# Kernel optimization log

Measured on AMD Instinct MI355X. Metric: run time of the kernel, lower is better.

## Reference

```python
import jax, jax.numpy as jnp
import numpy as np

SHAPELET_SIZE = 64
NUM_SHAPELETS = 128
IN_CHANNELS = 8


def setup_inputs() -> dict:
    key = jax.random.key(0)
    k1, k2 = jax.random.split(key)
    x = jax.random.normal(k1, (64, IN_CHANNELS, 2048), dtype=jnp.float32)
    shapelets = jax.random.normal(k2, (IN_CHANNELS, NUM_SHAPELETS, SHAPELET_SIZE), dtype=jnp.float32)
    return {"x": x, "shapelets": shapelets}


def _znorm(s):
    # Z-normalize along the time-step axis (dim 2), matching Znormalize_dim(shapelets, 2)
    mu = jnp.mean(s, axis=2, keepdims=True)
    sd = jnp.std(s, axis=2, keepdims=True)
    return (s - mu) / sd


def reference(x, shapelets):
    # x: (N, C, L); shapelets: (C, K, S)
    S = shapelets.shape[-1]
    N, C, L = x.shape
    W = L - S + 1
    # unfold(2, S, 1): sliding windows -> (N, C, W, S)
    idx = jnp.arange(W)[:, None] + jnp.arange(S)[None, :]  # (W, S)
    xw = x[:, :, idx]  # (N, C, W, S)
    sh = _znorm(shapelets)  # (C, K, S)
    # Euclidean cdist via ||a||^2 + ||b||^2 - 2 a.b (avoids (N,C,W,K,S) blowup)
    sq_x = jnp.sum(xw * xw, axis=-1)          # (N, C, W)
    sq_s = jnp.sum(sh * sh, axis=-1)          # (C, K)
    cross = jnp.einsum('ncws,cks->ncwk', xw, sh)  # (N, C, W, K)
    d2 = sq_x[..., None] + sq_s[None, :, None, :] - 2.0 * cross
    d = jnp.sqrt(jnp.maximum(d2, 1e-12))      # (N, C, W, K)
    # sum over channels, then global min over windows -> (N, 1, K)
    dsum = jnp.sum(d, axis=1)                 # (N, W, K)
    out = jnp.min(dsum, axis=1)[:, None, :]   # (N, 1, K)
    return out
```

## Files before the change

kernel.cpp:

```cpp
#include <hip/hip_runtime.h>
#include <math.h>

#define C 8
#define K 128
#define S 64
#define L 2048
#define NB 64
#define W (L - S + 1)
#define TW 128
#define NTW 16
#define XCS 200
#define XFS 200

typedef __attribute__((ext_vector_type(8))) short bf16x8;
typedef __attribute__((ext_vector_type(4))) float f32x4;

__device__ __forceinline__ unsigned short f2bf(float f) {
  unsigned int u = __float_as_uint(f);
  u += 0x7FFFu + ((u >> 16) & 1u);
  return (unsigned short)(u >> 16);
}

__global__ __launch_bounds__(256) void prep_kernel(const float* __restrict__ sh,
                                                   unsigned short* __restrict__ shzB,
                                                   float* __restrict__ sqs,
                                                   float* __restrict__ out) {
  int tid = blockIdx.x * 256 + threadIdx.x;
  if (tid < NB * K) out[tid] = __int_as_float(0x7F800000);
  int gid = blockIdx.x * 4 + (threadIdx.x >> 6);
  int lane = threadIdx.x & 63;
  float v = sh[(size_t)gid * S + lane];
  float s1 = v, s2 = v * v;
#pragma unroll
  for (int off = 32; off > 0; off >>= 1) {
    s1 += __shfl_down(s1, off);
    s2 += __shfl_down(s2, off);
  }
  s1 = __shfl(s1, 0);
  s2 = __shfl(s2, 0);
  float mu = s1 * (1.0f / S);
  float sd = sqrtf(fmaxf(s2 * (1.0f / S) - mu * mu, 0.0f));
  float z = (v - mu) / sd;
  int c = gid >> 7, k = gid & (K - 1), s = lane;
  int idx = c * 8192 + ((k >> 4) * 2 + (s >> 5)) * 512 +
            ((((s >> 3) & 3) * 16 + (k & 15)) * 8) + (s & 7);
  shzB[idx] = f2bf(z);
  float z2 = z * z;
#pragma unroll
  for (int off = 32; off > 0; off >>= 1) z2 += __shfl_down(z2, off);
  if (lane == 0) sqs[gid] = z2;
}

__global__ __launch_bounds__(256, 2) void main_kernel(const float* __restrict__ x,
                                                      const unsigned short* __restrict__ shzB,
                                                      const float* __restrict__ sqs,
                                                      int* __restrict__ out) {
  __shared__ __align__(16) unsigned short bbuf[2][8192];
  __shared__ __align__(16) unsigned short xcop[C][8][XCS];
  __shared__ __align__(16) float sqx[C][TW];

  const int t = threadIdx.x;
  const int lane = t & 63;
  const int wave = t >> 6;
  const int wgrp = wave >> 1;
  const int kgrp = wave & 1;
  const int col = lane & 15;
  const int quad = lane >> 4;
  const int n = blockIdx.y;
  const int w0 = blockIdx.x * TW;
  const float* xn = x + (size_t)n * C * L;

  {
    const unsigned short* g = shzB + t * 8;
    unsigned short* lb = &bbuf[0][wave * 512];
#pragma unroll
    for (int i = 0; i < 4; ++i)
      __builtin_amdgcn_global_load_lds(
          (const __attribute__((address_space(1))) void*)(g + i * 2048),
          (__attribute__((address_space(3))) void*)(lb + i * 2048), 16, 0, 0);
  }

  float* xf = (float*)&bbuf[1][0];
#pragma unroll
  for (int j = 0; j < 7; ++j) {
    int s = j * 256 + t;
    if (s < C * XFS) {
      int c = s / XFS, e = s - c * XFS;
      int g = w0 + e;
      xf[s] = (e < 192 && g < L) ? xn[c * L + g] : 0.0f;
    }
  }
  __syncthreads();

  {
    const int r = t >> 5, q = t & 31;
#pragma unroll
    for (int c = 0; c < C; ++c) {
#pragma unroll
      for (int j = 0; j < 3; ++j) {
        int i = (q + j * 32) * 2;
        int e = i + r;
        float f0 = xf[c * XFS + e];
        float f1 = xf[c * XFS + e + 1];
        unsigned int pk = (unsigned int)f2bf(f0) | ((unsigned int)f2bf(f1) << 16);
        *(unsigned int*)&xcop[c][r][i] = pk;
      }
    }
  }
  {
    int c = t >> 5, wl0 = (t & 31) << 2;
    const float* xr = xf + c * XFS;
    float s = 0.0f;
#pragma unroll
    for (int si = 0; si < S; ++si) { float v = xr[wl0 + si]; s = fmaf(v, v, s); }
    sqx[c][wl0] = s;
#pragma unroll
    for (int q = 1; q < 4; ++q) {
      float a = xr[wl0 + S - 1 + q], b = xr[wl0 + q - 1];
      s += a * a - b * b;
      sqx[c][wl0 + q] = s;
    }
  }
  __syncthreads();

  const f32x4 z4 = {0.0f, 0.0f, 0.0f, 0.0f};
  f32x4 dsum[4][4];
#pragma unroll
  for (int a = 0; a < 4; ++a)
#pragma unroll
    for (int b = 0; b < 4; ++b) dsum[a][b] = z4;

  const int m = col;
  const int r = m & 7;

  for (int c = 0; c < C; ++c) {
    if (c + 1 < C) {
      const unsigned short* g = shzB + (c + 1) * 8192 + t * 8;
      unsigned short* lb = &bbuf[(c + 1) & 1][wave * 512];
#pragma unroll
      for (int i = 0; i < 4; ++i)
        __builtin_amdgcn_global_load_lds(
            (const __attribute__((address_space(1))) void*)(g + i * 2048),
            (__attribute__((address_space(3))) void*)(lb + i * 2048), 16, 0, 0);
    }
    const unsigned short* bb = bbuf[c & 1];
    const unsigned short* xc = &xcop[c][0][0];

    f32x4 acc[4][4];
#pragma unroll
    for (int a = 0; a < 4; ++a)
#pragma unroll
      for (int b = 0; b < 4; ++b) acc[a][b] = z4;

#pragma unroll
    for (int ks = 0; ks < 2; ++ks) {
      bf16x8 bfr[4], afr[4];
#pragma unroll
      for (int kt = 0; kt < 4; ++kt)
        bfr[kt] = *(const bf16x8*)(bb + ((kgrp * 4 + kt) * 2 + ks) * 512 + lane * 8);
#pragma unroll
      for (int wt = 0; wt < 4; ++wt) {
        int i0 = wgrp * 64 + wt * 16 + m + ks * 32 + quad * 8 - r;
        afr[wt] = *(const bf16x8*)(xc + r * XCS + i0);
      }
#pragma unroll
      for (int wt = 0; wt < 4; ++wt)
#pragma unroll
        for (int kt = 0; kt < 4; ++kt)
          acc[wt][kt] = __builtin_amdgcn_mfma_f32_16x16x32_bf16(afr[wt], bfr[kt], acc[wt][kt], 0, 0, 0);
    }

    float sqsv[4];
#pragma unroll
    for (int kt = 0; kt < 4; ++kt) sqsv[kt] = sqs[c * K + kgrp * 64 + kt * 16 + col];
#pragma unroll
    for (int wt = 0; wt < 4; ++wt) {
      f32x4 sx = *(const f32x4*)&sqx[c][wgrp * 64 + wt * 16 + quad * 4];
#pragma unroll
      for (int kt = 0; kt < 4; ++kt) {
#pragma unroll
        for (int i = 0; i < 4; ++i) {
          float pre = sx[i] + sqsv[kt];
          float d2 = fmaf(-2.0f, acc[wt][kt][i], pre);
          dsum[wt][kt][i] += __builtin_amdgcn_sqrtf(fmaxf(d2, 1e-12f));
        }
      }
    }
    __syncthreads();
  }

  const float INF = __int_as_float(0x7F800000);
  int wbase = w0 + wgrp * 64;
#pragma unroll
  for (int kt = 0; kt < 4; ++kt) {
    float mv = INF;
#pragma unroll
    for (int wt = 0; wt < 4; ++wt)
#pragma unroll
      for (int i = 0; i < 4; ++i) {
        int w = wbase + wt * 16 + quad * 4 + i;
        float v = dsum[wt][kt][i];
        mv = (w < W) ? fminf(mv, v) : mv;
      }
    mv = fminf(mv, __shfl_xor(mv, 16));
    mv = fminf(mv, __shfl_xor(mv, 32));
    if (quad == 0)
      atomicMin(&out[n * K + kgrp * 64 + kt * 16 + col], __float_as_int(mv));
  }
}

extern "C" void kernel_launch(void* const* d_in, const int* in_sizes, int n_in,
                              void* d_out, int out_size, void* d_ws, size_t ws_size,
                              hipStream_t stream) {
  const float* x = (const float*)d_in[0];
  const float* sh = (const float*)d_in[1];
  float* out = (float*)d_out;
  unsigned short* shzB = (unsigned short*)d_ws;
  float* sqs = (float*)((char*)d_ws + C * K * S * 2);

  prep_kernel<<<256, 256, 0, stream>>>(sh, shzB, sqs, out);
  main_kernel<<<dim3(NTW, NB), 256, 0, stream>>>(x, shzB, sqs, (int*)out);
}
```

Measured before the change: 98.13 us.

## Load shapelet fragments from global into registers, widen blocks to 512 threads

Measured after the change: 187.2 us. +90.8%, slower.

```diff
diff --git a/kernel.cpp b/kernel.cpp
--- a/kernel.cpp
+++ b/kernel.cpp
@@ -44,168 +44,147 @@
   int c = gid >> 7, k = gid & (K - 1), s = lane;
   int idx = c * 8192 + ((k >> 4) * 2 + (s >> 5)) * 512 +
             ((((s >> 3) & 3) * 16 + (k & 15)) * 8) + (s & 7);
-  shzB[idx] = f2bf(z);
+  shzB[idx] = f2bf(-2.0f * z);
   float z2 = z * z;
 #pragma unroll
   for (int off = 32; off > 0; off >>= 1) z2 += __shfl_down(z2, off);
   if (lane == 0) sqs[gid] = z2;
 }
 
-__global__ __launch_bounds__(256, 2) void main_kernel(const float* __restrict__ x,
+__global__ __launch_bounds__(512, 4) void main_kernel(const float* __restrict__ x,
                                                       const unsigned short* __restrict__ shzB,
                                                       const float* __restrict__ sqs,
                                                       int* __restrict__ out) {
-  __shared__ __align__(16) unsigned short bbuf[2][8192];
   __shared__ __align__(16) unsigned short xcop[C][8][XCS];
   __shared__ __align__(16) float sqx[C][TW];
+  __shared__ __align__(16) float xf[C][XFS];
+  __shared__ __align__(16) float sqsl[C * K];
 
   const int t = threadIdx.x;
   const int lane = t & 63;
   const int wave = t >> 6;
-  const int wgrp = wave >> 1;
-  const int kgrp = wave & 1;
+  const int wgrp = wave & 1;
+  const int kgrp = wave >> 1;
   const int col = lane & 15;
   const int quad = lane >> 4;
   const int n = blockIdx.y;
   const int w0 = blockIdx.x * TW;
   const float* xn = x + (size_t)n * C * L;
 
-  {
-    const unsigned short* g = shzB + t * 8;
-    unsigned short* lb = &bbuf[0][wave * 512];
-#pragma unroll
-    for (int i = 0; i < 4; ++i)
-      __builtin_amdgcn_global_load_lds(
-          (const __attribute__((address_space(1))) void*)(g + i * 2048),
-          (__attribute__((address_space(3))) void*)(lb + i * 2048), 16, 0, 0);
-  }
-
-  float* xf = (float*)&bbuf[1][0];
-#pragma unroll
-  for (int j = 0; j < 7; ++j) {
-    int s = j * 256 + t;
+#pragma unroll
+  for (int j = 0; j < 4; ++j) {
+    int s = j * 512 + t;
     if (s < C * XFS) {
       int c = s / XFS, e = s - c * XFS;
       int g = w0 + e;
-      xf[s] = (e < 192 && g < L) ? xn[c * L + g] : 0.0f;
-    }
-  }
+      ((float*)xf)[s] = (e < 192 && g < L) ? xn[c * L + g] : 0.0f;
+    }
+  }
+  sqsl[t] = sqs[t];
+  sqsl[t + 512] = sqs[t + 512];
   __syncthreads();
 
   {
-    const int r = t >> 5, q = t & 31;
+    const int q = lane, r = wave;
 #pragma unroll
     for (int c = 0; c < C; ++c) {
-#pragma unroll
-      for (int j = 0; j < 3; ++j) {
-        int i = (q + j * 32) * 2;
-        int e = i + r;
-        float f0 = xf[c * XFS + e];
-        float f1 = xf[c * XFS + e + 1];
-        unsigned int pk = (unsigned int)f2bf(f0) | ((unsigned int)f2bf(f1) << 16);
+      {
+        int i = q * 2;
+        unsigned int pk = (unsigned int)f2bf(xf[c][i + r]) |
+                          ((unsigned int)f2bf(xf[c][i + r + 1]) << 16);
         *(unsigned int*)&xcop[c][r][i] = pk;
       }
+      if (q < 32) {
+        int i = 128 + q * 2;
+        unsigned int pk = (unsigned int)f2bf(xf[c][i + r]) |
+                          ((unsigned int)f2bf(xf[c][i + r + 1]) << 16);
+        *(unsigned int*)&xcop[c][r][i] = pk;
+      }
     }
   }
   {
-    int c = t >> 5, wl0 = (t & 31) << 2;
-    const float* xr = xf + c * XFS;
-    float s = 0.0f;
-#pragma unroll
-    for (int si = 0; si < S; ++si) { float v = xr[wl0 + si]; s = fmaf(v, v, s); }
-    sqx[c][wl0] = s;
-#pragma unroll
-    for (int q = 1; q < 4; ++q) {
-      float a = xr[wl0 + S - 1 + q], b = xr[wl0 + q - 1];
-      s += a * a - b * b;
-      sqx[c][wl0 + q] = s;
-    }
+    int c = t >> 6, wl = (t & 63) * 2;
+    const float* xr = xf[c];
+    float s0 = 0.0f;
+#pragma unroll
+    for (int si = 0; si < S; ++si) { float v = xr[wl + si]; s0 = fmaf(v, v, s0); }
+    sqx[c][wl] = s0;
+    float a = xr[wl + S], b = xr[wl];
+    sqx[c][wl + 1] = s0 + a * a - b * b;
   }
   __syncthreads();
 
   const f32x4 z4 = {0.0f, 0.0f, 0.0f, 0.0f};
-  f32x4 dsum[4][4];
+  f32x4 dsum[4][2];
 #pragma unroll
   for (int a = 0; a < 4; ++a)
 #pragma unroll
-    for (int b = 0; b < 4; ++b) dsum[a][b] = z4;
-
-  const int m = col;
-  const int r = m & 7;
-
+    for (int b = 0; b < 2; ++b) dsum[a][b] = z4;
+
+  const int r = col & 7;
+  const int abase = wgrp * 64 + (col - r) + quad * 8;
+  const unsigned short* bglob = shzB + (size_t)lane * 8;
+
+#pragma unroll
   for (int c = 0; c < C; ++c) {
-    if (c + 1 < C) {
-      const unsigned short* g = shzB + (c + 1) * 8192 + t * 8;
-      unsigned short* lb = &bbuf[(c + 1) & 1][wave * 512];
-#pragma unroll
-      for (int i = 0; i < 4; ++i)
-        __builtin_amdgcn_global_load_lds(
-            (const __attribute__((address_space(1))) void*)(g + i * 2048),
-            (__attribute__((address_space(3))) void*)(lb + i * 2048), 16, 0, 0);
-    }
-    const unsigned short* bb = bbuf[c & 1];
-    const unsigned short* xc = &xcop[c][0][0];
-
-    f32x4 acc[4][4];
-#pragma unroll
-    for (int a = 0; a < 4; ++a)
-#pragma unroll
-      for (int b = 0; b < 4; ++b) acc[a][b] = z4;
-
-#pragma unroll
-    for (int ks = 0; ks < 2; ++ks) {
-      bf16x8 bfr[4], afr[4];
-#pragma unroll
-      for (int kt = 0; kt < 4; ++kt)
-        bfr[kt] = *(const bf16x8*)(bb + ((kgrp * 4 + kt) * 2 + ks) * 512 + lane * 8);
-#pragma unroll
-      for (int wt = 0; wt < 4; ++wt) {
-        int i0 = wgrp * 64 + wt * 16 + m + ks * 32 + quad * 8 - r;
-        afr[wt] = *(const bf16x8*)(xc + r * XCS + i0);
-      }
-#pragma unroll
-      for (int wt = 0; wt < 4; ++wt)
-#pragma unroll
-        for (int kt = 0; kt < 4; ++kt)
-          acc[wt][kt] = __builtin_amdgcn_mfma_f32_16x16x32_bf16(afr[wt], bfr[kt], acc[wt][kt], 0, 0, 0);
-    }
-
-    float sqsv[4];
-#pragma unroll
-    for (int kt = 0; kt < 4; ++kt) sqsv[kt] = sqs[c * K + kgrp * 64 + kt * 16 + col];
+    bf16x8 bfr[2][2];
+#pragma unroll
+    for (int ks = 0; ks < 2; ++ks)
+#pragma unroll
+      for (int kt = 0; kt < 2; ++kt)
+        bfr[ks][kt] = *(const bf16x8*)(bglob + c * 8192 + ((kgrp * 2 + kt) * 2 + ks) * 512);
+
+    f32x4 acc[4][2];
+    float sq0 = sqsl[c * K + kgrp * 32 + col];
+    float sq1 = sqsl[c * K + kgrp * 32 + 16 + col];
 #pragma unroll
     for (int wt = 0; wt < 4; ++wt) {
       f32x4 sx = *(const f32x4*)&sqx[c][wgrp * 64 + wt * 16 + quad * 4];
 #pragma unroll
-      for (int kt = 0; kt < 4; ++kt) {
-#pragma unroll
-        for (int i = 0; i < 4; ++i) {
-          float pre = sx[i] + sqsv[kt];
-          float d2 = fmaf(-2.0f, acc[wt][kt][i], pre);
-          dsum[wt][kt][i] += __builtin_amdgcn_sqrtf(fmaxf(d2, 1e-12f));
-        }
-      }
-    }
-    __syncthreads();
+      for (int i = 0; i < 4; ++i) {
+        acc[wt][0][i] = sx[i] + sq0;
+        acc[wt][1][i] = sx[i] + sq1;
+      }
+    }
+
+#pragma unroll
+    for (int ks = 0; ks < 2; ++ks) {
+      bf16x8 afr[4];
+#pragma unroll
+      for (int wt = 0; wt < 4; ++wt)
+        afr[wt] = *(const bf16x8*)(&xcop[c][r][0] + abase + wt * 16 + ks * 32);
+#pragma unroll
+      for (int wt = 0; wt < 4; ++wt) {
+        acc[wt][0] = __builtin_amdgcn_mfma_f32_16x16x32_bf16(afr[wt], bfr[ks][0], acc[wt][0], 0, 0, 0);
+        acc[wt][1] = __builtin_amdgcn_mfma_f32_16x16x32_bf16(afr[wt], bfr[ks][1], acc[wt][1], 0, 0, 0);
+      }
+    }
+
+#pragma unroll
+    for (int wt = 0; wt < 4; ++wt)
+#pragma unroll
+      for (int kt = 0; kt < 2; ++kt)
+#pragma unroll
+        for (int i = 0; i < 4; ++i)
+          dsum[wt][kt][i] += __builtin_amdgcn_sqrtf(fmaxf(acc[wt][kt][i], 1e-12f));
   }
 
   const float INF = __int_as_float(0x7F800000);
   int wbase = w0 + wgrp * 64;
 #pragma unroll
-  for (int kt = 0; kt < 4; ++kt) {
+  for (int kt = 0; kt < 2; ++kt) {
     float mv = INF;
 #pragma unroll
     for (int wt = 0; wt < 4; ++wt)
 #pragma unroll
       for (int i = 0; i < 4; ++i) {
         int w = wbase + wt * 16 + quad * 4 + i;
-        float v = dsum[wt][kt][i];
-        mv = (w < W) ? fminf(mv, v) : mv;
+        mv = (w < W) ? fminf(mv, dsum[wt][kt][i]) : mv;
       }
     mv = fminf(mv, __shfl_xor(mv, 16));
     mv = fminf(mv, __shfl_xor(mv, 32));
     if (quad == 0)
-      atomicMin(&out[n * K + kgrp * 64 + kt * 16 + col], __float_as_int(mv));
+      atomicMin(&out[n * K + kgrp * 32 + kt * 16 + col], __float_as_int(mv));
   }
 }
 
@@ -219,5 +198,5 @@
   float* sqs = (float*)((char*)d_ws + C * K * S * 2);
 
   prep_kernel<<<256, 256, 0, stream>>>(sh, shzB, sqs, out);
-  main_kernel<<<dim3(NTW, NB), 256, 0, stream>>>(x, shzB, sqs, (int*)out);
-}
+  main_kernel<<<dim3(NTW, NB), 512, 0, stream>>>(x, shzB, sqs, (int*)out);
+}
```
